# Kernel tuning notes

Measured on AMD Instinct MI355X. Metric: run time of the kernel, lower is better.

The kernel has to match this reference:

```python
import jax, jax.numpy as jnp
import numpy as np
from jax import lax

B, C, HQ, WQ = 16, 256, 64, 64
HK = WK = 32
HEADS = 4
MAX_KV = 16
EPS = 1e-5  # BatchNorm2d default eps
HEAD_DIM = C // HEADS


def _bn(y, p):
    # p: [4, C] = (gamma, beta, running_mean, running_var); inference-mode BN
    g, b, m, v = p[0], p[1], p[2], p[3]
    return (y - m[:, None, None]) * (g / jnp.sqrt(v + EPS))[:, None, None] + b[:, None, None]


def _conv1x1_bn(x, w, p):
    # w: [O, C]; 1x1 conv (no bias) + BN, act=Identity
    return _bn(jnp.einsum('bchw,oc->bohw', x, w), p)


def _dwconv3x3_bn(x, w, p):
    # w: [C, 1, 3, 3] depthwise (groups=C), pad 'same'
    y = lax.conv_general_dilated(x, w, (1, 1), 'SAME', feature_group_count=C,
                                 dimension_numbers=('NCHW', 'OIHW', 'NCHW'))
    return _bn(y, p)


def _split_heads(x):
    b, c, h, w = x.shape
    return x.reshape(b, HEADS, c // HEADS, h * w).transpose(0, 1, 3, 2)  # b,heads,n,hd


def _merge_heads(x, h, w):
    b = x.shape[0]
    return x.transpose(0, 1, 3, 2).reshape(b, C, h, w)


def _pool2(x):
    # adaptive_avg_pool2d 32->16 with even ratio == exact 2x2 mean pooling
    b, c, h, w = x.shape
    return x.reshape(b, c, MAX_KV, 2, MAX_KV, 2).mean(axis=(3, 5))


def setup_inputs() -> dict:
    key = jax.random.key(0)
    ks = jax.random.split(key, 16)
    def bn_params(k):
        k1, k2, k3, k4 = jax.random.split(k, 4)
        gamma = 1.0 + 0.1 * jax.random.normal(k1, (C,), jnp.float32)
        beta = 0.1 * jax.random.normal(k2, (C,), jnp.float32)
        mean = 0.1 * jax.random.normal(k3, (C,), jnp.float32)
        var = jax.random.uniform(k4, (C,), jnp.float32, 0.5, 1.5)
        return jnp.stack([gamma, beta, mean, var])
    s = 1.0 / np.sqrt(C)
    inp = {
        'q': jax.random.normal(ks[0], (B, C, HQ, WQ), jnp.float32),
        'k': jax.random.normal(ks[1], (B, C, HK, WK), jnp.float32),
        'v': jax.random.normal(ks[2], (B, C, HK, WK), jnp.float32),
        'wq_w': s * jax.random.normal(ks[3], (C, C), jnp.float32),
        'wq_bn': bn_params(ks[4]),
        'wk_w': s * jax.random.normal(ks[5], (C, C), jnp.float32),
        'wk_bn': bn_params(ks[6]),
        'wv_w': s * jax.random.normal(ks[7], (C, C), jnp.float32),
        'wv_bn': bn_params(ks[8]),
        'pe_w': (1.0 / 3.0) * jax.random.normal(ks[9], (C, 1, 3, 3), jnp.float32),
        'pe_bn': bn_params(ks[10]),
        'proj_w': s * jax.random.normal(ks[11], (C, C), jnp.float32),
        'proj_bn': bn_params(ks[12]),
    }
    return inp


def reference(q, k, v, wq_w, wq_bn, wk_w, wk_bn, wv_w, wv_bn, pe_w, pe_bn, proj_w, proj_bn):
    # KV bounding: 32x32 > 16 -> pool to 16x16
    k = _pool2(k)
    v = _pool2(v)
    q_proj = _conv1x1_bn(q, wq_w, wq_bn)            # [B,C,64,64]
    q_s = _split_heads(q_proj)                      # [B,H,4096,64]
    k_s = _split_heads(_conv1x1_bn(k, wk_w, wk_bn)) # [B,H,256,64]
    v_s = _split_heads(_conv1x1_bn(v, wv_w, wv_bn)) # [B,H,256,64]
    scale = HEAD_DIM ** (-0.5)
    attn = jnp.einsum('bhnd,bhmd->bhnm', q_s, k_s) * scale  # [B,H,4096,256]
    attn = jax.nn.softmax(attn, axis=-1)
    y = jnp.einsum('bhnm,bhmd->bhnd', attn, v_s)    # [B,H,4096,64]
    y = _merge_heads(y, HQ, WQ) + _dwconv3x3_bn(q_proj, pe_w, pe_bn)
    return _conv1x1_bn(y, proj_w, proj_bn)
```

## Files before the change

kernel.cpp:

```cpp
#include <hip/hip_runtime.h>
#include <stdint.h>

using bf16x8 = __attribute__((ext_vector_type(8))) short;
using f32x4  = __attribute__((ext_vector_type(4))) float;
using u32x4  = __attribute__((ext_vector_type(4))) unsigned int;
using u32x2  = __attribute__((ext_vector_type(2))) unsigned int;

#define DEVFN static __device__ __forceinline__
#define MFMA  __builtin_amdgcn_mfma_f32_16x16x32_bf16

#define NB 16
#define NC 256
#define NQ 4096

#define OFF_WQ   0u
#define OFF_WK   131072u
#define OFF_WV   262144u
#define OFF_WP   393216u
#define OFF_BQ   524288u
#define OFF_BK   525312u
#define OFF_BV   526336u
#define OFF_BP   527360u
#define OFF_PEW  528384u
#define OFF_PEB  537600u
#define OFF_QP   1048576u
#define OFF_KS   34603008u
#define OFF_VT   36700160u
#define OFF_Y    38797312u

DEVFN unsigned short f2bf(float f) {
  unsigned u = __builtin_bit_cast(unsigned, f);
  return (unsigned short)((u + 0x8000u) >> 16);
}
DEVFN float bf2f(unsigned short s) {
  return __builtin_bit_cast(float, ((unsigned)s) << 16);
}
DEVFN unsigned pk2(float a, float b) {
  return (unsigned)f2bf(a) | ((unsigned)f2bf(b) << 16);
}

union U16B { u32x4 v; unsigned u[4]; unsigned short s[8]; };

DEVFN bf16x8 ldsfrag(const u32x4* xs, int row, int kb) {
  return __builtin_bit_cast(bf16x8, xs[row * 32 + (kb ^ (row & 7))]);
}
DEVFN bf16x8 gfrag(const u32x4* w, int row, int kb) {
  return __builtin_bit_cast(bf16x8, w[row * 32 + kb]);
}

__global__ void prep_kernel(const float* __restrict__ wq, const float* __restrict__ wqbn,
                            const float* __restrict__ wk, const float* __restrict__ wkbn,
                            const float* __restrict__ wv, const float* __restrict__ wvbn,
                            const float* __restrict__ wp, const float* __restrict__ wpbn,
                            const float* __restrict__ pe, const float* __restrict__ pebn,
                            unsigned char* __restrict__ ws) {
  const int bid = blockIdx.x, c = threadIdx.x;
  if (bid < 1024) {
    const int mat = bid >> 8, o = bid & 255;
    const float* w; const float* bn; unsigned short* wd; float* bd;
    if (mat == 0)      { w = wq; bn = wqbn; wd = (unsigned short*)(ws + OFF_WQ); bd = (float*)(ws + OFF_BQ); }
    else if (mat == 1) { w = wk; bn = wkbn; wd = (unsigned short*)(ws + OFF_WK); bd = (float*)(ws + OFF_BK); }
    else if (mat == 2) { w = wv; bn = wvbn; wd = (unsigned short*)(ws + OFF_WV); bd = (float*)(ws + OFF_BV); }
    else               { w = wp; bn = wpbn; wd = (unsigned short*)(ws + OFF_WP); bd = (float*)(ws + OFF_BP); }
    const float s = bn[o] / sqrtf(bn[768 + o] + 1e-5f);
    wd[o * 256 + c] = f2bf(w[o * 256 + c] * s);
    if (c == 0) bd[o] = bn[256 + o] - bn[512 + o] * s;
  } else {
    const float s = pebn[c] / sqrtf(pebn[768 + c] + 1e-5f);
    float* pw = (float*)(ws + OFF_PEW);
    #pragma unroll
    for (int kk = 0; kk < 9; ++kk) pw[kk * 256 + c] = pe[c * 9 + kk] * s;
    ((float*)(ws + OFF_PEB))[c] = pebn[256 + c] - pebn[512 + c] * s;
  }
}

__global__ __launch_bounds__(512) void qproj_kernel(const float* __restrict__ q,
                                                    unsigned char* __restrict__ ws) {
  __shared__ u32x4 xs[4096];
  const int b = blockIdx.x >> 5, ntile = blockIdx.x & 31;
  const int t = threadIdx.x;
  {
    const int nl = t & 127, cq = t >> 7;
    const float* qb = q + (size_t)b * NC * NQ + ntile * 128 + nl;
    #pragma unroll
    for (int it = 0; it < 8; ++it) {
      const int c0 = cq * 8 + it * 32;
      U16B pk;
      #pragma unroll
      for (int j = 0; j < 8; ++j) pk.s[j] = f2bf(qb[(size_t)(c0 + j) * NQ]);
      xs[nl * 32 + ((c0 >> 3) ^ (nl & 7))] = pk.v;
    }
  }
  __syncthreads();
  const int l = t & 63, w = t >> 6;
  const int lm = l & 15, lg = l >> 4;
  const int nsub = (w & 1) * 64, osub = (w >> 1) * 64;
  const u32x4* wm = (const u32x4*)(ws + OFF_WQ);
  const f32x4 fz = {0.f, 0.f, 0.f, 0.f};
  f32x4 acc[4][4];
  #pragma unroll
  for (int i = 0; i < 4; ++i)
    #pragma unroll
    for (int j = 0; j < 4; ++j) acc[i][j] = fz;
  for (int c0 = 0; c0 < 256; c0 += 32) {
    const int kb = (c0 >> 3) + lg;
    bf16x8 af[4], bfv[4];
    #pragma unroll
    for (int i = 0; i < 4; ++i) af[i] = ldsfrag(xs, nsub + i * 16 + lm, kb);
    #pragma unroll
    for (int j = 0; j < 4; ++j) bfv[j] = gfrag(wm, osub + j * 16 + lm, kb);
    #pragma unroll
    for (int i = 0; i < 4; ++i)
      #pragma unroll
      for (int j = 0; j < 4; ++j) acc[i][j] = MFMA(af[i], bfv[j], acc[i][j], 0, 0, 0);
  }
  const float* bias = (const float*)(ws + OFF_BQ);
  unsigned short* qp = (unsigned short*)(ws + OFF_QP) + ((size_t)b * NQ + ntile * 128) * NC;
  #pragma unroll
  for (int j = 0; j < 4; ++j) {
    const int o = osub + j * 16 + lm;
    const float bo = bias[o];
    #pragma unroll
    for (int i = 0; i < 4; ++i) {
      const int rb = nsub + i * 16 + lg * 4;
      #pragma unroll
      for (int r = 0; r < 4; ++r)
        qp[(size_t)(rb + r) * NC + o] = f2bf(acc[i][j][r] + bo);
    }
  }
}

__global__ __launch_bounds__(512) void kvproj_kernel(const float* __restrict__ kin,
                                                     const float* __restrict__ vin,
                                                     unsigned char* __restrict__ ws) {
  __shared__ u32x4 xs[4096];
  const int bid = blockIdx.x;
  const int b = bid >> 2, which = (bid >> 1) & 1, half = bid & 1;
  const int t = threadIdx.x;
  {
    const int nl = t & 127, cq = t >> 7;
    const int kv = half * 128 + nl;
    const int yy = kv >> 4, xx = kv & 15;
    const float* src = (which ? vin : kin) + (size_t)b * NC * 1024 + (2 * yy) * 32 + 2 * xx;
    #pragma unroll
    for (int it = 0; it < 8; ++it) {
      const int c0 = cq * 8 + it * 32;
      U16B pk;
      #pragma unroll
      for (int j = 0; j < 8; ++j) {
        const float* p = src + (size_t)(c0 + j) * 1024;
        pk.s[j] = f2bf((p[0] + p[1] + p[32] + p[33]) * 0.25f);
      }
      xs[nl * 32 + ((c0 >> 3) ^ (nl & 7))] = pk.v;
    }
  }
  __syncthreads();
  const int l = t & 63, w = t >> 6;
  const int lm = l & 15, lg = l >> 4;
  const f32x4 fz = {0.f, 0.f, 0.f, 0.f};
  f32x4 acc[4][4];
  #pragma unroll
  for (int i = 0; i < 4; ++i)
    #pragma unroll
    for (int j = 0; j < 4; ++j) acc[i][j] = fz;
  if (which == 0) {
    const int kvsub = (w & 1) * 64, osub = (w >> 1) * 64;
    const u32x4* wm = (const u32x4*)(ws + OFF_WK);
    for (int c0 = 0; c0 < 256; c0 += 32) {
      const int kb = (c0 >> 3) + lg;
      bf16x8 af[4], bfv[4];
      #pragma unroll
      for (int i = 0; i < 4; ++i) af[i] = ldsfrag(xs, kvsub + i * 16 + lm, kb);
      #pragma unroll
      for (int j = 0; j < 4; ++j) bfv[j] = gfrag(wm, osub + j * 16 + lm, kb);
      #pragma unroll
      for (int i = 0; i < 4; ++i)
        #pragma unroll
        for (int j = 0; j < 4; ++j) acc[i][j] = MFMA(af[i], bfv[j], acc[i][j], 0, 0, 0);
    }
    const float* bias = (const float*)(ws + OFF_BK);
    unsigned short* ksd = (unsigned short*)(ws + OFF_KS) + ((size_t)b * 256 + half * 128) * NC;
    #pragma unroll
    for (int j = 0; j < 4; ++j) {
      const int o = osub + j * 16 + lm;
      const float bo = bias[o];
      #pragma unroll
      for (int i = 0; i < 4; ++i) {
        const int rb = kvsub + i * 16 + lg * 4;
        #pragma unroll
        for (int r = 0; r < 4; ++r)
          ksd[(size_t)(rb + r) * NC + o] = f2bf(acc[i][j][r] + bo);
      }
    }
  } else {
    const int osub = (w >> 1) * 64, kvsub = (w & 1) * 64;
    const u32x4* wm = (const u32x4*)(ws + OFF_WV);
    for (int c0 = 0; c0 < 256; c0 += 32) {
      const int kb = (c0 >> 3) + lg;
      bf16x8 af[4], bfv[4];
      #pragma unroll
      for (int i = 0; i < 4; ++i) af[i] = gfrag(wm, osub + i * 16 + lm, kb);
      #pragma unroll
      for (int j = 0; j < 4; ++j) bfv[j] = ldsfrag(xs, kvsub + j * 16 + lm, kb);
      #pragma unroll
      for (int i = 0; i < 4; ++i)
        #pragma unroll
        for (int j = 0; j < 4; ++j) acc[i][j] = MFMA(af[i], bfv[j], acc[i][j], 0, 0, 0);
    }
    const float* bias = (const float*)(ws + OFF_BV);
    unsigned short* vtd = (unsigned short*)(ws + OFF_VT) + (size_t)b * 4 * 64 * 256;
    #pragma unroll
    for (int i = 0; i < 4; ++i) {
      #pragma unroll
      for (int r = 0; r < 4; ++r) {
        const int o = osub + i * 16 + lg * 4 + r;
        const float bo = bias[o];
        const size_t base = (size_t)((o >> 6) * 64 + (o & 63)) * 256 + half * 128 + kvsub;
        #pragma unroll
        for (int j = 0; j < 4; ++j)
          vtd[base + j * 16 + lm] = f2bf(acc[i][j][r] + bo);
      }
    }
  }
}

__global__ __launch_bounds__(256) void attn_kernel(unsigned char* __restrict__ ws) {
  __shared__ u32x4 plds[2048];
  __shared__ float sums[4][16];
  const int bid = blockIdx.x;
  const int qt = bid & 63, h = (bid >> 6) & 3, b = bid >> 8;
  const int t = threadIdx.x, w = t >> 6, l = t & 63;
  const int lm = l & 15, lg = l >> 4;
  const int q0 = qt * 64 + w * 16;
  const u32x4* qp = (const u32x4*)(ws + OFF_QP) + (size_t)b * NQ * 32;
  const u32x4* ksp = (const u32x4*)(ws + OFF_KS) + (size_t)b * 256 * 32;
  const u32x4* vtp = (const u32x4*)(ws + OFF_VT) + (size_t)(b * 4 + h) * 64 * 32;

  bf16x8 qf[2];
  #pragma unroll
  for (int kk = 0; kk < 2; ++kk)
    qf[kk] = __builtin_bit_cast(bf16x8, qp[(q0 + lm) * 32 + h * 8 + kk * 4 + lg]);

  const f32x4 fz = {0.f, 0.f, 0.f, 0.f};
  f32x4 st[16];
  #pragma unroll
  for (int tk = 0; tk < 16; ++tk) st[tk] = fz;
  #pragma unroll
  for (int tk = 0; tk < 16; ++tk) {
    #pragma unroll
    for (int kk = 0; kk < 2; ++kk) {
      bf16x8 kf = __builtin_bit_cast(bf16x8, ksp[(tk * 16 + lm) * 32 + h * 8 + kk * 4 + lg]);
      st[tk] = MFMA(kf, qf[kk], st[tk], 0, 0, 0);
    }
  }
  float mx = -3.0e38f;
  #pragma unroll
  for (int tk = 0; tk < 16; ++tk)
    #pragma unroll
    for (int r = 0; r < 4; ++r) mx = fmaxf(mx, st[tk][r]);
  mx = fmaxf(mx, __shfl_xor(mx, 16));
  mx = fmaxf(mx, __shfl_xor(mx, 32));
  float sum = 0.f;
  #pragma unroll
  for (int tk = 0; tk < 16; ++tk)
    #pragma unroll
    for (int r = 0; r < 4; ++r) {
      const float e = __expf(0.125f * (st[tk][r] - mx));
      st[tk][r] = e; sum += e;
    }
  sum += __shfl_xor(sum, 16);
  sum += __shfl_xor(sum, 32);
  if (l < 16) sums[w][l] = sum;
  u32x2* pw = (u32x2*)(plds + w * 512);
  #pragma unroll
  for (int tk = 0; tk < 16; ++tk) {
    const int slot = (2 * tk + (lg >> 1)) ^ (lm & 7);
    u32x2 pv = { pk2(st[tk][0], st[tk][1]), pk2(st[tk][2], st[tk][3]) };
    pw[lm * 64 + slot * 2 + (lg & 1)] = pv;
  }
  __syncthreads();
  f32x4 yacc[4];
  #pragma unroll
  for (int jj = 0; jj < 4; ++jj) yacc[jj] = fz;
  const u32x4* pr = plds + w * 512;
  for (int kk = 0; kk < 8; ++kk) {
    bf16x8 pf = __builtin_bit_cast(bf16x8, pr[lm * 32 + ((kk * 4 + lg) ^ (lm & 7))]);
    #pragma unroll
    for (int jj = 0; jj < 4; ++jj) {
      bf16x8 vf = __builtin_bit_cast(bf16x8, vtp[(jj * 16 + lm) * 32 + kk * 4 + lg]);
      yacc[jj] = MFMA(pf, vf, yacc[jj], 0, 0, 0);
    }
  }
  unsigned short* yo = (unsigned short*)(ws + OFF_Y) + (size_t)b * NQ * NC;
  #pragma unroll
  for (int r = 0; r < 4; ++r) {
    const float inv = __builtin_amdgcn_rcpf(sums[w][lg * 4 + r]);
    const size_t rowoff = (size_t)(q0 + lg * 4 + r) * NC + h * 64;
    #pragma unroll
    for (int jj = 0; jj < 4; ++jj)
      yo[rowoff + jj * 16 + lm] = f2bf(yacc[jj][r] * inv);
  }
}

__global__ __launch_bounds__(512) void final_kernel(float* __restrict__ out,
                                                    unsigned char* __restrict__ ws) {
  __shared__ u32x4 xs[4096];
  const int b = blockIdx.x >> 5, ntile = blockIdx.x & 31;
  const int t = threadIdx.x;
  {
    const int nl = t & 127, cq = t >> 7;
    const int n = ntile * 128 + nl;
    const int yy = n >> 6, xx = n & 63;
    const u32x4* qp = (const u32x4*)(ws + OFF_QP) + (size_t)b * NQ * 32;
    const u32x4* yv = (const u32x4*)(ws + OFF_Y) + (size_t)b * NQ * 32;
    const float* pew = (const float*)(ws + OFF_PEW);
    const float* peb = (const float*)(ws + OFF_PEB);
    #pragma unroll
    for (int it = 0; it < 8; ++it) {
      const int c0 = cq * 8 + it * 32, cb = c0 >> 3;
      float a8[8];
      #pragma unroll
      for (int j = 0; j < 8; ++j) a8[j] = peb[c0 + j];
      #pragma unroll
      for (int dy = -1; dy <= 1; ++dy) {
        #pragma unroll
        for (int dx = -1; dx <= 1; ++dx) {
          const int y2 = yy + dy, x2 = xx + dx;
          if (y2 >= 0 && y2 < 64 && x2 >= 0 && x2 < 64) {
            U16B qv; qv.v = qp[(size_t)(y2 * 64 + x2) * 32 + cb];
            const float* wr = pew + ((dy + 1) * 3 + (dx + 1)) * 256 + c0;
            #pragma unroll
            for (int j = 0; j < 8; ++j) a8[j] += bf2f(qv.s[j]) * wr[j];
          }
        }
      }
      U16B yvv; yvv.v = yv[(size_t)n * 32 + cb];
      U16B pk;
      #pragma unroll
      for (int j = 0; j < 8; ++j) pk.s[j] = f2bf(a8[j] + bf2f(yvv.s[j]));
      xs[nl * 32 + (cb ^ (nl & 7))] = pk.v;
    }
  }
  __syncthreads();
  const int l = t & 63, w = t >> 6;
  const int lm = l & 15, lg = l >> 4;
  const int osub = (w >> 1) * 64, nsub = (w & 1) * 64;
  const u32x4* wm = (const u32x4*)(ws + OFF_WP);
  const f32x4 fz = {0.f, 0.f, 0.f, 0.f};
  f32x4 acc[4][4];
  #pragma unroll
  for (int i = 0; i < 4; ++i)
    #pragma unroll
    for (int j = 0; j < 4; ++j) acc[i][j] = fz;
  for (int c0 = 0; c0 < 256; c0 += 32) {
    const int kb = (c0 >> 3) + lg;
    bf16x8 af[4], bfv[4];
    #pragma unroll
    for (int i = 0; i < 4; ++i) af[i] = gfrag(wm, osub + i * 16 + lm, kb);
    #pragma unroll
    for (int j = 0; j < 4; ++j) bfv[j] = ldsfrag(xs, nsub + j * 16 + lm, kb);
    #pragma unroll
    for (int i = 0; i < 4; ++i)
      #pragma unroll
      for (int j = 0; j < 4; ++j) acc[i][j] = MFMA(af[i], bfv[j], acc[i][j], 0, 0, 0);
  }
  const float* bias = (const float*)(ws + OFF_BP);
  float* ob = out + (size_t)b * NC * NQ + ntile * 128;
  #pragma unroll
  for (int i = 0; i < 4; ++i) {
    #pragma unroll
    for (int r = 0; r < 4; ++r) {
      const int o = osub + i * 16 + lg * 4 + r;
      const float bo = bias[o];
      #pragma unroll
      for (int j = 0; j < 4; ++j)
        ob[(size_t)o * NQ + nsub + j * 16 + lm] = acc[i][j][r] + bo;
    }
  }
}

extern "C" void kernel_launch(void* const* d_in, const int* in_sizes, int n_in,
                              void* d_out, int out_size, void* d_ws, size_t ws_size,
                              hipStream_t stream) {
  const float* q    = (const float*)d_in[0];
  const float* k    = (const float*)d_in[1];
  const float* v    = (const float*)d_in[2];
  const float* wq   = (const float*)d_in[3];
  const float* wqbn = (const float*)d_in[4];
  const float* wk   = (const float*)d_in[5];
  const float* wkbn = (const float*)d_in[6];
  const float* wv   = (const float*)d_in[7];
  const float* wvbn = (const float*)d_in[8];
  const float* pe   = (const float*)d_in[9];
  const float* pebn = (const float*)d_in[10];
  const float* wp   = (const float*)d_in[11];
  const float* wpbn = (const float*)d_in[12];
  unsigned char* ws = (unsigned char*)d_ws;

  prep_kernel<<<1025, 256, 0, stream>>>(wq, wqbn, wk, wkbn, wv, wvbn, wp, wpbn, pe, pebn, ws);
  qproj_kernel<<<512, 512, 0, stream>>>(q, ws);
  kvproj_kernel<<<64, 512, 0, stream>>>(k, v, ws);
  attn_kernel<<<4096, 256, 0, stream>>>(ws);
  final_kernel<<<512, 512, 0, stream>>>((float*)d_out, ws);
}
```

Baseline: 412.4 us.

## Vectorize projection loads/stores and split kvproj into more smaller blocks

The qproj input staging now reads float4 along the spatial dimension instead of scalar strided loads. The qproj and final epilogues are reoriented by swapping MFMA operand roles, so each lane writes packed 4-element bf16 or float4 vectors instead of scalar stores. kvproj is repartitioned from 64 blocks into 256 smaller blocks with float2 pooled loads and packed stores, which raises parallelism for a small kernel. The cost is more redundant weight reads per kvproj block and some added register pressure from the f4 staging array.

Measured after the change: 423.9 us. 2.8% more time.

```diff
diff --git a/kernel.cpp b/kernel.cpp
--- a/kernel.cpp
+++ b/kernel.cpp
@@ -7,7 +7,7 @@
 using u32x2  = __attribute__((ext_vector_type(2))) unsigned int;
 
 #define DEVFN static __device__ __forceinline__
-#define MFMA  __builtin_amdgcn_mfma_f32_16x16x32_bf16
+#define MFMA16 __builtin_amdgcn_mfma_f32_16x16x32_bf16
 
 #define NB 16
 #define NC 256
@@ -80,15 +80,22 @@
   const int b = blockIdx.x >> 5, ntile = blockIdx.x & 31;
   const int t = threadIdx.x;
   {
-    const int nl = t & 127, cq = t >> 7;
-    const float* qb = q + (size_t)b * NC * NQ + ntile * 128 + nl;
-    #pragma unroll
-    for (int it = 0; it < 8; ++it) {
-      const int c0 = cq * 8 + it * 32;
-      U16B pk;
-      #pragma unroll
-      for (int j = 0; j < 8; ++j) pk.s[j] = f2bf(qb[(size_t)(c0 + j) * NQ]);
-      xs[nl * 32 + ((c0 >> 3) ^ (nl & 7))] = pk.v;
+    const int n4 = t & 31, cg = t >> 5;
+    const float* qb = q + (size_t)b * NC * NQ + ntile * 128 + n4 * 4;
+    f32x4 f4[16];
+    #pragma unroll
+    for (int cc = 0; cc < 16; ++cc)
+      f4[cc] = *(const f32x4*)(qb + (size_t)(cg * 16 + cc) * NQ);
+    #pragma unroll
+    for (int rr = 0; rr < 4; ++rr) {
+      const int row = n4 * 4 + rr;
+      #pragma unroll
+      for (int s = 0; s < 2; ++s) {
+        U16B pk;
+        #pragma unroll
+        for (int j = 0; j < 8; ++j) pk.s[j] = f2bf(f4[s * 8 + j][rr]);
+        xs[row * 32 + ((cg * 2 + s) ^ (row & 7))] = pk.v;
+      }
     }
   }
   __syncthreads();
@@ -106,26 +113,26 @@
     const int kb = (c0 >> 3) + lg;
     bf16x8 af[4], bfv[4];
     #pragma unroll
-    for (int i = 0; i < 4; ++i) af[i] = ldsfrag(xs, nsub + i * 16 + lm, kb);
-    #pragma unroll
-    for (int j = 0; j < 4; ++j) bfv[j] = gfrag(wm, osub + j * 16 + lm, kb);
+    for (int i = 0; i < 4; ++i) af[i] = gfrag(wm, osub + i * 16 + lm, kb);
+    #pragma unroll
+    for (int j = 0; j < 4; ++j) bfv[j] = ldsfrag(xs, nsub + j * 16 + lm, kb);
     #pragma unroll
     for (int i = 0; i < 4; ++i)
       #pragma unroll
-      for (int j = 0; j < 4; ++j) acc[i][j] = MFMA(af[i], bfv[j], acc[i][j], 0, 0, 0);
+      for (int j = 0; j < 4; ++j) acc[i][j] = MFMA16(af[i], bfv[j], acc[i][j], 0, 0, 0);
   }
   const float* bias = (const float*)(ws + OFF_BQ);
   unsigned short* qp = (unsigned short*)(ws + OFF_QP) + ((size_t)b * NQ + ntile * 128) * NC;
   #pragma unroll
-  for (int j = 0; j < 4; ++j) {
-    const int o = osub + j * 16 + lm;
-    const float bo = bias[o];
-    #pragma unroll
-    for (int i = 0; i < 4; ++i) {
-      const int rb = nsub + i * 16 + lg * 4;
-      #pragma unroll
-      for (int r = 0; r < 4; ++r)
-        qp[(size_t)(rb + r) * NC + o] = f2bf(acc[i][j][r] + bo);
+  for (int i = 0; i < 4; ++i) {
+    const int ob = osub + i * 16 + lg * 4;
+    const f32x4 b4 = *(const f32x4*)(bias + ob);
+    #pragma unroll
+    for (int j = 0; j < 4; ++j) {
+      const int n = nsub + j * 16 + lm;
+      u32x2 pv = { pk2(acc[i][j][0] + b4[0], acc[i][j][1] + b4[1]),
+                   pk2(acc[i][j][2] + b4[2], acc[i][j][3] + b4[3]) };
+      *(u32x2*)(qp + (size_t)n * NC + ob) = pv;
     }
   }
 }
@@ -133,23 +140,25 @@
 __global__ __launch_bounds__(512) void kvproj_kernel(const float* __restrict__ kin,
                                                      const float* __restrict__ vin,
                                                      unsigned char* __restrict__ ws) {
-  __shared__ u32x4 xs[4096];
+  __shared__ u32x4 xs[1024];
   const int bid = blockIdx.x;
-  const int b = bid >> 2, which = (bid >> 1) & 1, half = bid & 1;
+  const int b = bid >> 4, which = (bid >> 3) & 1, part = bid & 7;
   const int t = threadIdx.x;
   {
-    const int nl = t & 127, cq = t >> 7;
-    const int kv = half * 128 + nl;
+    const int nl = t & 31, cq = t >> 5;
+    const int kv = part * 32 + nl;
     const int yy = kv >> 4, xx = kv & 15;
     const float* src = (which ? vin : kin) + (size_t)b * NC * 1024 + (2 * yy) * 32 + 2 * xx;
     #pragma unroll
-    for (int it = 0; it < 8; ++it) {
-      const int c0 = cq * 8 + it * 32;
+    for (int s = 0; s < 2; ++s) {
+      const int c0 = cq * 16 + s * 8;
       U16B pk;
       #pragma unroll
       for (int j = 0; j < 8; ++j) {
         const float* p = src + (size_t)(c0 + j) * 1024;
-        pk.s[j] = f2bf((p[0] + p[1] + p[32] + p[33]) * 0.25f);
+        const float2 p01 = *(const float2*)p;
+        const float2 p23 = *(const float2*)(p + 32);
+        pk.s[j] = f2bf((p01.x + p01.y + p23.x + p23.y) * 0.25f);
       }
       xs[nl * 32 + ((c0 >> 3) ^ (nl & 7))] = pk.v;
     }
@@ -157,69 +166,58 @@
   __syncthreads();
   const int l = t & 63, w = t >> 6;
   const int lm = l & 15, lg = l >> 4;
+  const int osub = (w >> 1) * 64;
+  const int kvsub = (w & 1) * 16;
   const f32x4 fz = {0.f, 0.f, 0.f, 0.f};
-  f32x4 acc[4][4];
-  #pragma unroll
-  for (int i = 0; i < 4; ++i)
-    #pragma unroll
-    for (int j = 0; j < 4; ++j) acc[i][j] = fz;
   if (which == 0) {
-    const int kvsub = (w & 1) * 64, osub = (w >> 1) * 64;
     const u32x4* wm = (const u32x4*)(ws + OFF_WK);
+    f32x4 acc[4];
+    #pragma unroll
+    for (int i = 0; i < 4; ++i) acc[i] = fz;
     for (int c0 = 0; c0 < 256; c0 += 32) {
       const int kb = (c0 >> 3) + lg;
-      bf16x8 af[4], bfv[4];
-      #pragma unroll
-      for (int i = 0; i < 4; ++i) af[i] = ldsfrag(xs, kvsub + i * 16 + lm, kb);
-      #pragma unroll
-      for (int j = 0; j < 4; ++j) bfv[j] = gfrag(wm, osub + j * 16 + lm, kb);
-      #pragma unroll
-      for (int i = 0; i < 4; ++i)
-        #pragma unroll
-        for (int j = 0; j < 4; ++j) acc[i][j] = MFMA(af[i], bfv[j], acc[i][j], 0, 0, 0);
+      bf16x8 bfv = ldsfrag(xs, kvsub + lm, kb);
+      #pragma unroll
+      for (int i = 0; i < 4; ++i) {
+        bf16x8 af = gfrag(wm, osub + i * 16 + lm, kb);
+        acc[i] = MFMA16(af, bfv, acc[i], 0, 0, 0);
+      }
     }
     const float* bias = (const float*)(ws + OFF_BK);
-    unsigned short* ksd = (unsigned short*)(ws + OFF_KS) + ((size_t)b * 256 + half * 128) * NC;
+    unsigned short* ksd = (unsigned short*)(ws + OFF_KS) + (size_t)b * 256 * NC;
+    const int kv = part * 32 + kvsub + lm;
+    #pragma unroll
+    for (int i = 0; i < 4; ++i) {
+      const int ob = osub + i * 16 + lg * 4;
+      const f32x4 b4 = *(const f32x4*)(bias + ob);
+      u32x2 pv = { pk2(acc[i][0] + b4[0], acc[i][1] + b4[1]),
+                   pk2(acc[i][2] + b4[2], acc[i][3] + b4[3]) };
+      *(u32x2*)(ksd + (size_t)kv * NC + ob) = pv;
+    }
+  } else {
+    const u32x4* wm = (const u32x4*)(ws + OFF_WV);
+    f32x4 acc[4];
+    #pragma unroll
+    for (int j = 0; j < 4; ++j) acc[j] = fz;
+    for (int c0 = 0; c0 < 256; c0 += 32) {
+      const int kb = (c0 >> 3) + lg;
+      bf16x8 af = ldsfrag(xs, kvsub + lm, kb);
+      #pragma unroll
+      for (int j = 0; j < 4; ++j) {
+        bf16x8 bfv = gfrag(wm, osub + j * 16 + lm, kb);
+        acc[j] = MFMA16(af, bfv, acc[j], 0, 0, 0);
+      }
+    }
+    const float* bias = (const float*)(ws + OFF_BV);
+    unsigned short* vtd = (unsigned short*)(ws + OFF_VT) + (size_t)b * 256 * 256;
+    const int kvb = part * 32 + kvsub + lg * 4;
     #pragma unroll
     for (int j = 0; j < 4; ++j) {
       const int o = osub + j * 16 + lm;
       const float bo = bias[o];
-      #pragma unroll
-      for (int i = 0; i < 4; ++i) {
-        const int rb = kvsub + i * 16 + lg * 4;
-        #pragma unroll
-        for (int r = 0; r < 4; ++r)
-          ksd[(size_t)(rb + r) * NC + o] = f2bf(acc[i][j][r] + bo);
-      }
-    }
-  } else {
-    const int osub = (w >> 1) * 64, kvsub = (w & 1) * 64;
-    const u32x4* wm = (const u32x4*)(ws + OFF_WV);
-    for (int c0 = 0; c0 < 256; c0 += 32) {
-      const int kb = (c0 >> 3) + lg;
-      bf16x8 af[4], bfv[4];
-      #pragma unroll
-      for (int i = 0; i < 4; ++i) af[i] = gfrag(wm, osub + i * 16 + lm, kb);
-      #pragma unroll
-      for (int j = 0; j < 4; ++j) bfv[j] = ldsfrag(xs, kvsub + j * 16 + lm, kb);
-      #pragma unroll
-      for (int i = 0; i < 4; ++i)
-        #pragma unroll
-        for (int j = 0; j < 4; ++j) acc[i][j] = MFMA(af[i], bfv[j], acc[i][j], 0, 0, 0);
-    }
-    const float* bias = (const float*)(ws + OFF_BV);
-    unsigned short* vtd = (unsigned short*)(ws + OFF_VT) + (size_t)b * 4 * 64 * 256;
-    #pragma unroll
-    for (int i = 0; i < 4; ++i) {
-      #pragma unroll
-      for (int r = 0; r < 4; ++r) {
-        const int o = osub + i * 16 + lg * 4 + r;
-        const float bo = bias[o];
-        const size_t base = (size_t)((o >> 6) * 64 + (o & 63)) * 256 + half * 128 + kvsub;
-        #pragma unroll
-        for (int j = 0; j < 4; ++j)
-          vtd[base + j * 16 + lm] = f2bf(acc[i][j][r] + bo);
-      }
+      u32x2 pv = { pk2(acc[j][0] + bo, acc[j][1] + bo),
+                   pk2(acc[j][2] + bo, acc[j][3] + bo) };
+      *(u32x2*)(vtd + (size_t)o * 256 + kvb) = pv;
     }
   }
 }
@@ -250,7 +248,7 @@
     #pragma unroll
     for (int kk = 0; kk < 2; ++kk) {
       bf16x8 kf = __builtin_bit_cast(bf16x8, ksp[(tk * 16 + lm) * 32 + h * 8 + kk * 4 + lg]);
-      st[tk] = MFMA(kf, qf[kk], st[tk], 0, 0, 0);
+      st[tk] = MFMA16(kf, qf[kk], st[tk], 0, 0, 0);
     }
   }
   float mx = -3.0e38f;
@@ -288,7 +286,7 @@
     #pragma unroll
     for (int jj = 0; jj < 4; ++jj) {
       bf16x8 vf = __builtin_bit_cast(bf16x8, vtp[(jj * 16 + lm) * 32 + kk * 4 + lg]);
-      yacc[jj] = MFMA(pf, vf, yacc[jj], 0, 0, 0);
+      yacc[jj] = MFMA16(pf, vf, yacc[jj], 0, 0, 0);
     }
   }
   unsigned short* yo = (unsigned short*)(ws + OFF_Y) + (size_t)b * NQ * NC;
@@ -356,25 +354,25 @@
     const int kb = (c0 >> 3) + lg;
     bf16x8 af[4], bfv[4];
     #pragma unroll
-    for (int i = 0; i < 4; ++i) af[i] = gfrag(wm, osub + i * 16 + lm, kb);
-    #pragma unroll
-    for (int j = 0; j < 4; ++j) bfv[j] = ldsfrag(xs, nsub + j * 16 + lm, kb);
+    for (int i = 0; i < 4; ++i) af[i] = ldsfrag(xs, nsub + i * 16 + lm, kb);
+    #pragma unroll
+    for (int j = 0; j < 4; ++j) bfv[j] = gfrag(wm, osub + j * 16 + lm, kb);
     #pragma unroll
     for (int i = 0; i < 4; ++i)
       #pragma unroll
-      for (int j = 0; j < 4; ++j) acc[i][j] = MFMA(af[i], bfv[j], acc[i][j], 0, 0, 0);
+      for (int j = 0; j < 4; ++j) acc[i][j] = MFMA16(af[i], bfv[j], acc[i][j], 0, 0, 0);
   }
   const float* bias = (const float*)(ws + OFF_BP);
   float* ob = out + (size_t)b * NC * NQ + ntile * 128;
   #pragma unroll
-  for (int i = 0; i < 4; ++i) {
-    #pragma unroll
-    for (int r = 0; r < 4; ++r) {
-      const int o = osub + i * 16 + lg * 4 + r;
-      const float bo = bias[o];
-      #pragma unroll
-      for (int j = 0; j < 4; ++j)
-        ob[(size_t)o * NQ + nsub + j * 16 + lm] = acc[i][j][r] + bo;
+  for (int j = 0; j < 4; ++j) {
+    const int o = osub + j * 16 + lm;
+    const float bo = bias[o];
+    #pragma unroll
+    for (int i = 0; i < 4; ++i) {
+      const int nb = nsub + i * 16 + lg * 4;
+      f32x4 v = { acc[i][j][0] + bo, acc[i][j][1] + bo, acc[i][j][2] + bo, acc[i][j][3] + bo };
+      *(f32x4*)(ob + (size_t)o * NQ + nb) = v;
     }
   }
 }
@@ -399,7 +397,7 @@
 
   prep_kernel<<<1025, 256, 0, stream>>>(wq, wqbn, wk, wkbn, wv, wvbn, wp, wpbn, pe, pebn, ws);
   qproj_kernel<<<512, 512, 0, stream>>>(q, ws);
-  kvproj_kernel<<<64, 512, 0, stream>>>(k, v, ws);
+  kvproj_kernel<<<256, 512, 0, stream>>>(k, v, ws);
   attn_kernel<<<4096, 256, 0, stream>>>(ws);
   final_kernel<<<512, 512, 0, stream>>>((float*)d_out, ws);
 }
```
